# Kernel tuning notes

Hardware: AMD Instinct MI355X
Metric: run time of the kernel (lower is better)

## Reference

```python
import jax, jax.numpy as jnp
import numpy as np

SIGMA = 0.1   # sigma_disc (params[3])
ALPHA = 0.05  # alpha_disc (params[2])


def setup_inputs() -> dict:
    key = jax.random.key(0)
    k1, k2, k3 = jax.random.split(key, 3)
    E, S, T = 3, 8192, 100  # num_events, num_samples, num_bin + num_extra_bin
    logits = jax.random.normal(k1, (E, S, T), dtype=jnp.float32)
    event_out = jax.nn.softmax(logits, axis=-1)  # per-event discrete hazard probs, rows sum to 1
    event_times = jax.random.randint(k2, (S, E), 0, 99).astype(jnp.int32)
    labs = jax.random.randint(k3, (S, E), 0, 2).astype(jnp.int32)
    return {"event_out": event_out, "event_times": event_times, "labs": labs,
            "num_bin": 96, "num_extra_bin": 4}


def _c_loss(event_out, event_times, labs, T):
    # cum[e, k, t] = sum(event_out[e, k, :t+1]); risk with cutoff c = 1 - cum[..., c-1]
    cum = jnp.cumsum(event_out, axis=-1)  # (E, S, T)
    E = event_out.shape[0]
    penalty = jnp.float32(0.0)
    for i in range(E):  # small fixed number of events
        c = cum[i]                    # (S, T)
        t = event_times[:, i]         # (S,)
        lab = labs[:, i]              # (S,)
        had = lab == 1
        # ---- forward concordance (had_event branch) ----
        e_f = jnp.minimum(t + 1, T - 1)              # per-reference-sample cutoff, >= 1
        # risk_f[j, k] = 1 - sum(event_out[k, :e_f[j]]) = 1 - cum[k, e_f[j]-1]
        risk_f = 1.0 - c[:, e_f - 1].T               # (S_j, S_k)
        diff_f = risk_f - jnp.diagonal(risk_f)[:, None]  # comp_risk - reference_risk
        # f_compare: t_k > e_j - 1  OR  (t_k == e_j - 1 AND lab_k == 0)
        mask_f = had[:, None] & ((t[None, :] >= e_f[:, None]) |
                                 ((t[None, :] == e_f[:, None] - 1) & (lab[None, :] == 0)))
        penalty = penalty + jnp.sum(jnp.where(mask_f & (diff_f < 0),
                                              jnp.exp(-diff_f / SIGMA), 0.0))
        # ---- backward concordance (back_c branch, active when t_j > 0) ----
        e_b = jnp.minimum(jnp.where(had, t, t + 1), T - 1)
        risk_b = 1.0 - c[:, jnp.maximum(e_b, 1) - 1].T
        diff_b = risk_b - jnp.diagonal(risk_b)[:, None]
        # b_compare: t_k <= e_j - 1 AND lab_k == 1
        mask_b = (t > 0)[:, None] & (t[None, :] <= e_b[:, None] - 1) & (lab[None, :] == 1)
        penalty = penalty + jnp.sum(jnp.where(mask_b & (diff_b > 0),
                                              jnp.exp(diff_b / SIGMA), 0.0))
    return ALPHA * penalty


def reference(event_out, event_times, labs, num_bin, num_extra_bin):
    return _c_loss(event_out, event_times, labs, num_bin + num_extra_bin)
```

## Files before the change

kernel.cpp:

```cpp
#include <hip/hip_runtime.h>

#define E_CONST 3
#define T_CONST 100
#define C10 10.0f
#define ALPHA_C 0.05f
#define SPLIT 4
#define MAXK 8192
#define NGROUP (E_CONST * 2 * T_CONST)

__device__ inline int waveInclScan(int v, int lane) {
    #pragma unroll
    for (int off = 1; off < 64; off <<= 1) {
        int n = __shfl_up(v, off, 64);
        if (lane >= off) v += n;
    }
    return v;
}

__global__ __launch_bounds__(512) void prep_kernel(
    const float* __restrict__ event_out, float* __restrict__ cumT, int S)
{
    __shared__ float tile[64][101];
    const int tid = threadIdx.x;
    const int rowbase = (int)blockIdx.x * 64;
    const float4* __restrict__ src =
        reinterpret_cast<const float4*>(event_out) + (size_t)rowbase * 25;
    for (int idx = tid; idx < 64 * 25; idx += 512) {
        const float4 v = src[idx];
        const int r = idx / 25;
        const int c = idx - r * 25;
        float* d = &tile[r][c * 4];
        d[0] = v.x; d[1] = v.y; d[2] = v.z; d[3] = v.w;
    }
    __syncthreads();
    if (tid < 64) {
        float run = 0.f;
        #pragma unroll 4
        for (int c = 0; c < T_CONST; ++c) { run += tile[tid][c]; tile[tid][c] = run; }
    }
    __syncthreads();
    const int i  = rowbase / S;
    const int s0 = rowbase - i * S;
    float* __restrict__ dst = cumT + (size_t)i * T_CONST * S + s0;
    for (int idx = tid; idx < 64 * T_CONST; idx += 512) {
        const int t = idx >> 6;
        const int r = idx & 63;
        dst[(size_t)t * S + r] = tile[r][t];
    }
}

__global__ __launch_bounds__(256) void thrfill_kernel(
    const float* __restrict__ cumT, const int* __restrict__ et,
    const int* __restrict__ labs, float* __restrict__ thrVals,
    int* __restrict__ gCnt, int S)
{
    const int lane = threadIdx.x & 63;
    const int gid = (int)blockIdx.x * 4 + (threadIdx.x >> 6);
    const int i = gid / 200;
    const int r = gid - i * 200;
    const int dir = r / 100;
    const int tt = r - dir * 100;

    int colIdx = tt, t1, l1, t2 = -1, l2 = 0;
    bool any = true;
    if (dir == 0) { t1 = tt; l1 = 1; }
    else {
        const int cb = tt;
        if (cb >= T_CONST - 1) any = false;
        t1 = cb + 1; l1 = 1;
        if (cb > 0) { t2 = cb; l2 = 0; }
    }

    int cnt = 0;
    if (any) {
        const float* __restrict__ col = cumT + ((size_t)i * T_CONST + colIdx) * S;
        float* __restrict__ dst = thrVals + (size_t)gid * MAXK;
        for (int s0 = 0; s0 < S; s0 += 256) {
            int tsv[4], lsv[4];
            #pragma unroll
            for (int j = 0; j < 4; ++j) {
                const int s = s0 + j * 64 + lane;
                tsv[j] = et[s * E_CONST + i];
                lsv[j] = labs[s * E_CONST + i];
            }
            #pragma unroll
            for (int j = 0; j < 4; ++j) {
                const int s = s0 + j * 64 + lane;
                const bool pred = ((tsv[j] == t1) & (lsv[j] == l1)) ||
                                  ((t2 >= 0) & (tsv[j] == t2) & (lsv[j] == l2));
                const unsigned long long mask = __ballot(pred);
                if (pred) {
                    const int off = __popcll(mask & ((1ull << lane) - 1ull));
                    dst[cnt + off] = __expf(C10 * col[s]);
                }
                cnt += (int)__popcll(mask);
            }
        }
    }
    if (lane == 0) gCnt[gid] = cnt;
}

__global__ __launch_bounds__(256) void grouppair_kernel(
    const float* __restrict__ cumT, const float* __restrict__ thrVals,
    const int* __restrict__ gCnt, const int* __restrict__ et,
    const int* __restrict__ labs, float* __restrict__ partials, int S)
{
    __shared__ __align__(16) float elds[2048];
    __shared__ float wsum[4];
    __shared__ int wcnt[4];
    __shared__ int nTot;
    const int tid = threadIdx.x;
    const int lane = tid & 63, wid = tid >> 6;

    int x = (int)blockIdx.x;
    const int sp = x & (SPLIT - 1); x >>= 2;
    const int dir = x & 1;          x >>= 1;
    const int tt = x % T_CONST;
    const int i  = x / T_CONST;

    int colIdx = 0, tref = 0, tgid = 0;
    bool active = true;
    if (dir == 0) { colIdx = tt; tref = tt; tgid = i * 200 + tt; }
    else {
        const int cb = (T_CONST - 2) - tt;
        if (cb < 0) active = false;
        else { colIdx = cb; tref = cb; tgid = i * 200 + 100 + cb; }
    }
    const int K = active ? gCnt[tgid] : 0;
    if (K <= 0) active = false;

    float blocktot = 0.f;
    if (active) {
        const float* __restrict__ col = cumT + ((size_t)i * T_CONST + colIdx) * S;
        const float sgn = (dir == 0) ? C10 : -C10;
        const int chunk = S / SPLIT;
        const int cbeg = sp * chunk;

        float ev[8];
        int mask = 0, m = 0;
        #pragma unroll
        for (int j = 0; j < 8; ++j) {
            const int s = cbeg + tid + j * 256;
            const int ts = et[s * E_CONST + i];
            const int ls = labs[s * E_CONST + i];
            const bool mem = (dir == 0)
                ? ((ts > tref) | ((ts == tref) & (ls == 0)))
                : ((ts <= tref) & (ls == 1));
            ev[j] = __expf(sgn * col[s]);
            if (mem) { mask |= (1 << j); ++m; }
        }
        const int incl = waveInclScan(m, lane);
        if (lane == 63) wcnt[wid] = incl;
        __syncthreads();
        int off = 0;
        for (int w = 0; w < wid; ++w) off += wcnt[w];
        int base = incl - m + off;
        #pragma unroll
        for (int j = 0; j < 8; ++j)
            if (mask & (1 << j)) elds[base++] = ev[j];
        if (tid == 255) {
            nTot = base;
            const int np = (base + 3) & ~3;
            for (int p = base; p < np; ++p) elds[p] = 0.f;
        }
        __syncthreads();

        const int n = nTot;
        if (n > 0) {
            const int qn4 = ((n + 3) & ~3) >> 2;
            const int kq = tid & 31;
            const int ep = tid >> 5;
            const float4* __restrict__ e4 = reinterpret_cast<const float4*>(elds);
            const float* __restrict__ tv = thrVals + (size_t)tgid * MAXK;
            const int nkc = (K + 31) >> 5;

            for (int kc = 0; kc < nkc; ++kc) {
                const int j = (kc << 5) + kq;
                float thr = 1e30f, factor = 0.f;
                if (j < K) {
                    const float tval = tv[j];
                    if (dir == 0) { thr = tval;        factor = 1.0f / tval; }
                    else          { thr = 1.0f / tval; factor = tval; }
                }
                float acc = 0.f;
                for (int q = ep; q < qn4; q += 8) {
                    const float4 v = e4[q];
                    acc += (v.x > thr) ? v.x : 0.f;
                    acc += (v.y > thr) ? v.y : 0.f;
                    acc += (v.z > thr) ? v.z : 0.f;
                    acc += (v.w > thr) ? v.w : 0.f;
                }
                blocktot += acc * factor;
            }
        }
    }

    for (int off = 32; off > 0; off >>= 1) blocktot += __shfl_down(blocktot, off, 64);
    if (lane == 0) wsum[wid] = blocktot;
    __syncthreads();
    if (tid == 0) partials[blockIdx.x] = wsum[0] + wsum[1] + wsum[2] + wsum[3];
}

__global__ __launch_bounds__(1024) void reduce_kernel(
    const float* __restrict__ partials, int n, float* __restrict__ out)
{
    const int tid = threadIdx.x;
    float s0 = 0.f, s1 = 0.f, s2 = 0.f, s3 = 0.f;
    const int n4 = n & ~3;
    for (int idx = tid * 4; idx < n4; idx += 4096) {
        const float4 v = *reinterpret_cast<const float4*>(partials + idx);
        s0 += v.x; s1 += v.y; s2 += v.z; s3 += v.w;
    }
    for (int idx = n4 + tid; idx < n; idx += 1024) s0 += partials[idx];
    float sum = (s0 + s1) + (s2 + s3);
    for (int off = 32; off > 0; off >>= 1) sum += __shfl_down(sum, off, 64);
    __shared__ float wsum[16];
    const int lane = tid & 63, wd = tid >> 6;
    if (lane == 0) wsum[wd] = sum;
    __syncthreads();
    if (tid == 0) {
        float t = 0.f;
        for (int w = 0; w < 16; ++w) t += wsum[w];
        out[0] = ALPHA_C * t;
    }
}

__global__ __launch_bounds__(64) void prep_fb_kernel(
    const float* __restrict__ event_out, const int* __restrict__ et,
    const int* __restrict__ labs, float* __restrict__ cumT,
    int* __restrict__ tlA, int S)
{
    const int gid = blockIdx.x * 64 + threadIdx.x;
    const int i = gid / S;
    const int s = gid - i * S;
    const float4* __restrict__ row =
        reinterpret_cast<const float4*>(event_out + (size_t)gid * T_CONST);
    float* __restrict__ base = cumT + (size_t)i * T_CONST * S + s;
    float run = 0.f;
    #pragma unroll
    for (int c = 0; c < T_CONST / 4; ++c) {
        const float4 v = row[c];
        const float c0 = run + v.x;
        const float c1 = c0 + v.y;
        const float c2 = c1 + v.z;
        const float c3 = c2 + v.w;
        base[(size_t)(4 * c + 0) * S] = c0;
        base[(size_t)(4 * c + 1) * S] = c1;
        base[(size_t)(4 * c + 2) * S] = c2;
        base[(size_t)(4 * c + 3) * S] = c3;
        run = c3;
    }
    const int t   = et[s * E_CONST + i];
    const int lab = labs[s * E_CONST + i];
    tlA[i * S + s] = (t & 0xffff) | (lab << 16);
}

__global__ __launch_bounds__(256) void pair_fb_kernel(
    const float* __restrict__ cumT, const int* __restrict__ tlA,
    float* __restrict__ partials, int S)
{
    const int bx = blockIdx.x;
    const int i = bx / S;
    const int k = bx - i * S;
    const int base = i * S;
    const int tlk = tlA[base + k];
    const int t_k = tlk & 0xffff;
    const int lab_k = tlk >> 16;
    const bool doF = (lab_k == 1);
    const bool doB = (t_k > 0);
    float sum = 0.f;
    if (doF || doB) {
        const int cb = lab_k ? (t_k > 0 ? t_k - 1 : 0) : t_k;
        const float* __restrict__ colF = cumT + ((size_t)i * T_CONST + t_k) * S;
        const float* __restrict__ colB = cumT + ((size_t)i * T_CONST + cb)  * S;
        const float vf_k = colF[k];
        const float vb_k = colB[k];
        const int* __restrict__ tlp = tlA + base;
        for (int s = threadIdx.x; s < S; s += 256) {
            const int tls = tlp[s];
            const int t_s = tls & 0xffff;
            const int lab_s = tls >> 16;
            if (doF) {
                const float vs = colF[s];
                const bool c = (t_s > t_k) | ((t_s == t_k) & (lab_s == 0));
                if (c & (vs > vf_k)) sum += __expf((vs - vf_k) * C10);
            }
            if (doB) {
                const float vs = colB[s];
                const bool c = (t_s <= cb) & (lab_s == 1);
                if (c & (vb_k > vs)) sum += __expf((vb_k - vs) * C10);
            }
        }
    }
    for (int off = 32; off > 0; off >>= 1) sum += __shfl_down(sum, off, 64);
    __shared__ float wsum[4];
    const int lane = threadIdx.x & 63, wd = threadIdx.x >> 6;
    if (lane == 0) wsum[wd] = sum;
    __syncthreads();
    if (threadIdx.x == 0) partials[bx] = wsum[0] + wsum[1] + wsum[2] + wsum[3];
}

extern "C" void kernel_launch(void* const* d_in, const int* in_sizes, int n_in,
                              void* d_out, int out_size, void* d_ws, size_t ws_size,
                              hipStream_t stream)
{
    const float* event_out = (const float*)d_in[0];
    const int*   et        = (const int*)d_in[1];
    const int*   labsp     = (const int*)d_in[2];
    const int S = in_sizes[1] / E_CONST;

    const size_t colElems = (size_t)E_CONST * T_CONST * S;
    const size_t esElems  = (size_t)E_CONST * S;
    const int    gpBlocks = E_CONST * T_CONST * 2 * SPLIT;

    char* p = (char*)d_ws;
    float* cumT     = (float*)p; p += colElems * 4;
    float* thrVals  = (float*)p; p += (size_t)NGROUP * MAXK * 4;
    int*   gCnt     = (int*)p;   p += (size_t)NGROUP * 4;
    float* partials = (float*)p; p += (size_t)gpBlocks * 4;
    const size_t needed = (size_t)(p - (char*)d_ws);
    const size_t fallback_needed = colElems * 4 + esElems * 4 * 2;

    const int prepBlocks = (E_CONST * S) / 64;

    if (ws_size >= needed && (E_CONST * S) % 64 == 0 &&
        (S / SPLIT) == 2048 && (S % 256) == 0 && S <= MAXK) {
        hipLaunchKernelGGL(prep_kernel, dim3(prepBlocks), dim3(512), 0, stream,
                           event_out, cumT, S);
        hipLaunchKernelGGL(thrfill_kernel, dim3(NGROUP / 4), dim3(256), 0, stream,
                           cumT, et, labsp, thrVals, gCnt, S);
        hipLaunchKernelGGL(grouppair_kernel, dim3(gpBlocks), dim3(256), 0, stream,
                           cumT, thrVals, gCnt, et, labsp, partials, S);
        hipLaunchKernelGGL(reduce_kernel, dim3(1), dim3(1024), 0, stream,
                           partials, gpBlocks, (float*)d_out);
    } else if (ws_size >= fallback_needed) {
        const int nB = E_CONST * S;
        float* cumT2     = (float*)d_ws;
        int*   tlA2      = (int*)(cumT2 + colElems);
        float* partials2 = (float*)(tlA2 + esElems);
        hipLaunchKernelGGL(prep_fb_kernel, dim3(E_CONST * S / 64), dim3(64), 0, stream,
                           event_out, et, labsp, cumT2, tlA2, S);
        hipLaunchKernelGGL(pair_fb_kernel, dim3(nB), dim3(256), 0, stream,
                           cumT2, tlA2, partials2, S);
        hipLaunchKernelGGL(reduce_kernel, dim3(1), dim3(1024), 0, stream,
                           partials2, nB, (float*)d_out);
    }
}
```

Before: 131.9 us.

## Merge prep and threshold-fill kernels, computing cumsums directly from event_out

Combines the transpose/cumsum prep kernel and the threshold-fill kernel into one launch. The fill blocks no longer depend on cumT: each matching sample re-sums its own row prefix from event_out. This removes a launch and the serial dependency between the two stages. In exchange, the fill path does redundant per-lane prefix sums with divergent, uncoalesced row reads, and it reads et/labs one wave-width at a time instead of four.

```diff
diff --git a/kernel.cpp b/kernel.cpp
--- a/kernel.cpp
+++ b/kernel.cpp
@@ -17,84 +17,93 @@
     return v;
 }
 
-__global__ __launch_bounds__(512) void prep_kernel(
-    const float* __restrict__ event_out, float* __restrict__ cumT, int S)
+__global__ __launch_bounds__(512) void combo_kernel(
+    const float* __restrict__ event_out, const int* __restrict__ et,
+    const int* __restrict__ labs, float* __restrict__ cumT,
+    float* __restrict__ thrVals, int* __restrict__ gCnt,
+    int prepBlocks, int S)
 {
     __shared__ float tile[64][101];
     const int tid = threadIdx.x;
-    const int rowbase = (int)blockIdx.x * 64;
-    const float4* __restrict__ src =
-        reinterpret_cast<const float4*>(event_out) + (size_t)rowbase * 25;
-    for (int idx = tid; idx < 64 * 25; idx += 512) {
-        const float4 v = src[idx];
-        const int r = idx / 25;
-        const int c = idx - r * 25;
-        float* d = &tile[r][c * 4];
-        d[0] = v.x; d[1] = v.y; d[2] = v.z; d[3] = v.w;
-    }
-    __syncthreads();
-    if (tid < 64) {
-        float run = 0.f;
-        #pragma unroll 4
-        for (int c = 0; c < T_CONST; ++c) { run += tile[tid][c]; tile[tid][c] = run; }
-    }
-    __syncthreads();
-    const int i  = rowbase / S;
-    const int s0 = rowbase - i * S;
-    float* __restrict__ dst = cumT + (size_t)i * T_CONST * S + s0;
-    for (int idx = tid; idx < 64 * T_CONST; idx += 512) {
-        const int t = idx >> 6;
-        const int r = idx & 63;
-        dst[(size_t)t * S + r] = tile[r][t];
-    }
-}
-
-__global__ __launch_bounds__(256) void thrfill_kernel(
-    const float* __restrict__ cumT, const int* __restrict__ et,
-    const int* __restrict__ labs, float* __restrict__ thrVals,
-    int* __restrict__ gCnt, int S)
-{
-    const int lane = threadIdx.x & 63;
-    const int gid = (int)blockIdx.x * 4 + (threadIdx.x >> 6);
+
+    if ((int)blockIdx.x < prepBlocks) {
+        const int rowbase = (int)blockIdx.x * 64;
+        const float4* __restrict__ src =
+            reinterpret_cast<const float4*>(event_out) + (size_t)rowbase * 25;
+        for (int idx = tid; idx < 64 * 25; idx += 512) {
+            const float4 v = src[idx];
+            const int r = idx / 25;
+            const int c = idx - r * 25;
+            float* d = &tile[r][c * 4];
+            d[0] = v.x; d[1] = v.y; d[2] = v.z; d[3] = v.w;
+        }
+        __syncthreads();
+        if (tid < 64) {
+            float run = 0.f;
+            #pragma unroll 4
+            for (int c = 0; c < T_CONST; ++c) { run += tile[tid][c]; tile[tid][c] = run; }
+        }
+        __syncthreads();
+        const int i  = rowbase / S;
+        const int s0 = rowbase - i * S;
+        float* __restrict__ dst = cumT + (size_t)i * T_CONST * S + s0;
+        for (int idx = tid; idx < 64 * T_CONST; idx += 512) {
+            const int t = idx >> 6;
+            const int r = idx & 63;
+            dst[(size_t)t * S + r] = tile[r][t];
+        }
+        return;
+    }
+
+    const int lane = tid & 63;
+    const int gid = ((int)blockIdx.x - prepBlocks) * 8 + (tid >> 6);
+    if (gid >= NGROUP) return;
     const int i = gid / 200;
     const int r = gid - i * 200;
     const int dir = r / 100;
     const int tt = r - dir * 100;
 
-    int colIdx = tt, t1, l1, t2 = -1, l2 = 0;
+    const int colIdx = tt;
+    int t1 = 0, t2 = -1;
     bool any = true;
-    if (dir == 0) { t1 = tt; l1 = 1; }
+    if (dir == 0) { t1 = tt; }
     else {
         const int cb = tt;
         if (cb >= T_CONST - 1) any = false;
-        t1 = cb + 1; l1 = 1;
-        if (cb > 0) { t2 = cb; l2 = 0; }
+        t1 = cb + 1;
+        if (cb > 0) t2 = cb;
     }
 
     int cnt = 0;
     if (any) {
-        const float* __restrict__ col = cumT + ((size_t)i * T_CONST + colIdx) * S;
         float* __restrict__ dst = thrVals + (size_t)gid * MAXK;
-        for (int s0 = 0; s0 < S; s0 += 256) {
-            int tsv[4], lsv[4];
-            #pragma unroll
-            for (int j = 0; j < 4; ++j) {
-                const int s = s0 + j * 64 + lane;
-                tsv[j] = et[s * E_CONST + i];
-                lsv[j] = labs[s * E_CONST + i];
+        const int nfull = (colIdx + 1) >> 2;
+        const int rem   = (colIdx + 1) & 3;
+        for (int s0 = 0; s0 < S; s0 += 64) {
+            const int s = s0 + lane;
+            const int ts = et[s * E_CONST + i];
+            const int ls = labs[s * E_CONST + i];
+            const bool pred = ((ts == t1) & (ls == 1)) |
+                              ((t2 >= 0) & (ts == t2) & (ls == 0));
+            const unsigned long long mask = __ballot(pred);
+            if (pred) {
+                const int off = __popcll(mask & ((1ull << lane) - 1ull));
+                const float4* __restrict__ row4 = reinterpret_cast<const float4*>(
+                    event_out + ((size_t)i * S + s) * T_CONST);
+                float run = 0.f;
+                for (int c = 0; c < nfull; ++c) {
+                    const float4 v = row4[c];
+                    run += v.x; run += v.y; run += v.z; run += v.w;
+                }
+                if (rem) {
+                    const float4 v = row4[nfull];
+                    run += v.x;
+                    if (rem > 1) run += v.y;
+                    if (rem > 2) run += v.z;
+                }
+                dst[cnt + off] = __expf(C10 * run);
             }
-            #pragma unroll
-            for (int j = 0; j < 4; ++j) {
-                const int s = s0 + j * 64 + lane;
-                const bool pred = ((tsv[j] == t1) & (lsv[j] == l1)) ||
-                                  ((t2 >= 0) & (tsv[j] == t2) & (lsv[j] == l2));
-                const unsigned long long mask = __ballot(pred);
-                if (pred) {
-                    const int off = __popcll(mask & ((1ull << lane) - 1ull));
-                    dst[cnt + off] = __expf(C10 * col[s]);
-                }
-                cnt += (int)__popcll(mask);
-            }
+            cnt += (int)__popcll(mask);
         }
     }
     if (lane == 0) gCnt[gid] = cnt;
@@ -322,13 +331,13 @@
     const size_t fallback_needed = colElems * 4 + esElems * 4 * 2;
 
     const int prepBlocks = (E_CONST * S) / 64;
+    const int thrBlocks  = NGROUP / 8;
 
     if (ws_size >= needed && (E_CONST * S) % 64 == 0 &&
         (S / SPLIT) == 2048 && (S % 256) == 0 && S <= MAXK) {
-        hipLaunchKernelGGL(prep_kernel, dim3(prepBlocks), dim3(512), 0, stream,
-                           event_out, cumT, S);
-        hipLaunchKernelGGL(thrfill_kernel, dim3(NGROUP / 4), dim3(256), 0, stream,
-                           cumT, et, labsp, thrVals, gCnt, S);
+        hipLaunchKernelGGL(combo_kernel, dim3(prepBlocks + thrBlocks), dim3(512), 0, stream,
+                           event_out, et, labsp, cumT, thrVals, gCnt,
+                           prepBlocks, S);
         hipLaunchKernelGGL(grouppair_kernel, dim3(gpBlocks), dim3(256), 0, stream,
                            cumT, thrVals, gCnt, et, labsp, partials, S);
         hipLaunchKernelGGL(reduce_kernel, dim3(1), dim3(1024), 0, stream,
```

New measurement: 431.0 us. 227% more time.

## Use one block per group in threshold fill with block-wide scan compaction

Applied to the files above, without the earlier changes.

The threshold-fill kernel now gives each (event, direction, bin) group a whole 256-thread block instead of a single wave. Each thread loads four consecutive cumulative values as a float4 and compacts matches with a wave scan plus a shared-memory prefix across waves. This spreads the serial per-wave scan over the S samples across more threads and vectorizes the column load. The cost is two block barriers per 1024-sample chunk, an exp computed even for non-matching samples, and strided uncoalesced loads of the times and labels.

```diff
diff --git a/kernel.cpp b/kernel.cpp
--- a/kernel.cpp
+++ b/kernel.cpp
@@ -54,50 +54,59 @@
     const int* __restrict__ labs, float* __restrict__ thrVals,
     int* __restrict__ gCnt, int S)
 {
-    const int lane = threadIdx.x & 63;
-    const int gid = (int)blockIdx.x * 4 + (threadIdx.x >> 6);
+    __shared__ int wcnt[4];
+    const int tid = threadIdx.x;
+    const int lane = tid & 63, wid = tid >> 6;
+    const int gid = (int)blockIdx.x;
     const int i = gid / 200;
     const int r = gid - i * 200;
     const int dir = r / 100;
     const int tt = r - dir * 100;
 
-    int colIdx = tt, t1, l1, t2 = -1, l2 = 0;
+    const int colIdx = tt;
+    int t1 = 0, t2 = -1;
     bool any = true;
-    if (dir == 0) { t1 = tt; l1 = 1; }
+    if (dir == 0) { t1 = tt; }
     else {
         const int cb = tt;
         if (cb >= T_CONST - 1) any = false;
-        t1 = cb + 1; l1 = 1;
-        if (cb > 0) { t2 = cb; l2 = 0; }
+        t1 = cb + 1;
+        if (cb > 0) t2 = cb;
     }
 
     int cnt = 0;
     if (any) {
         const float* __restrict__ col = cumT + ((size_t)i * T_CONST + colIdx) * S;
         float* __restrict__ dst = thrVals + (size_t)gid * MAXK;
-        for (int s0 = 0; s0 < S; s0 += 256) {
-            int tsv[4], lsv[4];
+        for (int s0 = 0; s0 < S; s0 += 1024) {
+            const int sb = s0 + tid * 4;
+            const float4 cv = *reinterpret_cast<const float4*>(col + sb);
+            float tv[4]; int mask = 0, m = 0;
             #pragma unroll
             for (int j = 0; j < 4; ++j) {
-                const int s = s0 + j * 64 + lane;
-                tsv[j] = et[s * E_CONST + i];
-                lsv[j] = labs[s * E_CONST + i];
+                const int s = sb + j;
+                const int ts = et[s * E_CONST + i];
+                const int ls = labs[s * E_CONST + i];
+                const float c = (j == 0) ? cv.x : (j == 1) ? cv.y
+                              : (j == 2) ? cv.z : cv.w;
+                tv[j] = __expf(C10 * c);
+                const bool p = ((ts == t1) & (ls == 1)) |
+                               ((t2 >= 0) & (ts == t2) & (ls == 0));
+                if (p) { mask |= (1 << j); ++m; }
             }
+            const int incl = waveInclScan(m, lane);
+            if (lane == 63) wcnt[wid] = incl;
+            __syncthreads();
+            int base = cnt + incl - m;
+            for (int w = 0; w < wid; ++w) base += wcnt[w];
             #pragma unroll
-            for (int j = 0; j < 4; ++j) {
-                const int s = s0 + j * 64 + lane;
-                const bool pred = ((tsv[j] == t1) & (lsv[j] == l1)) ||
-                                  ((t2 >= 0) & (tsv[j] == t2) & (lsv[j] == l2));
-                const unsigned long long mask = __ballot(pred);
-                if (pred) {
-                    const int off = __popcll(mask & ((1ull << lane) - 1ull));
-                    dst[cnt + off] = __expf(C10 * col[s]);
-                }
-                cnt += (int)__popcll(mask);
-            }
-        }
-    }
-    if (lane == 0) gCnt[gid] = cnt;
+            for (int j = 0; j < 4; ++j)
+                if (mask & (1 << j)) dst[base++] = tv[j];
+            cnt += wcnt[0] + wcnt[1] + wcnt[2] + wcnt[3];
+            __syncthreads();
+        }
+    }
+    if (tid == 0) gCnt[gid] = cnt;
 }
 
 __global__ __launch_bounds__(256) void grouppair_kernel(
@@ -324,10 +333,10 @@
     const int prepBlocks = (E_CONST * S) / 64;
 
     if (ws_size >= needed && (E_CONST * S) % 64 == 0 &&
-        (S / SPLIT) == 2048 && (S % 256) == 0 && S <= MAXK) {
+        (S / SPLIT) == 2048 && (S % 1024) == 0 && S <= MAXK) {
         hipLaunchKernelGGL(prep_kernel, dim3(prepBlocks), dim3(512), 0, stream,
                            event_out, cumT, S);
-        hipLaunchKernelGGL(thrfill_kernel, dim3(NGROUP / 4), dim3(256), 0, stream,
+        hipLaunchKernelGGL(thrfill_kernel, dim3(NGROUP), dim3(256), 0, stream,
                            cumT, et, labsp, thrVals, gCnt, S);
         hipLaunchKernelGGL(grouppair_kernel, dim3(gpBlocks), dim3(256), 0, stream,
                            cumT, thrVals, gCnt, et, labsp, partials, S);
```

Result: faster. 116.0 us (-12.0%).
